# Kernel optimization log

Measured on AMD Instinct MI355X. Metric: run time of the kernel, lower is better.

Reference implementation:

```python
import jax, jax.numpy as jnp
import numpy as np

N = 64      # features
L = 96      # history length
LP = 24     # prediction length
H = 128     # rnn hidden
B = 1024    # batch


def setup_inputs() -> dict:
    key = jax.random.key(0)
    ks = jax.random.split(key, 16)
    # monotonically increasing timestamps
    tp_all = jnp.cumsum(jax.random.uniform(ks[0], (B, L + LP), dtype=jnp.float32), axis=1)
    tp_true = tp_all[:, :L]
    tp_pred = tp_all[:, L:]
    X = jax.random.normal(ks[1], (B, L, N), dtype=jnp.float32)
    mask = jax.random.randint(ks[2], (B, L, N), 0, 2).astype(jnp.float32)
    def unif(k, shape, fan):
        std = 1.0 / np.sqrt(fan)
        return jax.random.uniform(k, shape, jnp.float32, -std, std)
    # TemporalDecay for h: W (H,N), b (H); std = 1/sqrt(out)
    Wh_dec = unif(ks[3], (H, N), H)
    bh_dec = unif(ks[4], (H,), H)
    # TemporalDecay for x (diag): W (N,N) but only diagonal used
    Wx_dec = unif(ks[5], (N, N), N)
    bx_dec = unif(ks[6], (N,), N)
    # GRUCell: input size = 2N + H
    in_sz = 2 * N + H
    W_ih = unif(ks[7], (3 * H, in_sz), H)
    W_hh = unif(ks[8], (3 * H, H), H)
    b_ih = unif(ks[9], (3 * H,), H)
    b_hh = unif(ks[10], (3 * H,), H)
    # output projection
    Wp = unif(ks[11], (N, H), H)
    bp = unif(ks[12], (N,), H)
    return {"tp_pred": tp_pred, "X": X, "tp_true": tp_true, "mask": mask,
            "Wh_dec": Wh_dec, "bh_dec": bh_dec, "Wx_dec": Wx_dec, "bx_dec": bx_dec,
            "W_ih": W_ih, "W_hh": W_hh, "b_ih": b_ih, "b_hh": b_hh,
            "Wp": Wp, "bp": bp}


def _grud(tp_pred, X, tp_true, mask, Wh_dec, bh_dec, Wx_dec, bx_dec,
          W_ih, W_hh, b_ih, b_hh, Wp, bp):
    Bsz, Lh, Nf = X.shape
    Lp = tp_pred.shape[1]
    Lall = Lh + Lp
    Hh = Wh_dec.shape[0]

    # pad future with zeros (unobserved)
    X_all = jnp.concatenate([X, jnp.zeros((Bsz, Lp, Nf), X.dtype)], axis=1)
    M_all = jnp.concatenate([mask, jnp.zeros((Bsz, Lp, Nf), X.dtype)], axis=1)
    tp = jnp.concatenate([tp_true, tp_pred], axis=1)

    # deltas: first-difference padded with 0 at t=0, broadcast over features
    dt = jnp.pad(tp[:, 1:] - tp[:, :-1], ((0, 0), (1, 0)))  # (B, Lall)
    deltas = jnp.broadcast_to(dt[:, :, None], (Bsz, Lall, Nf))

    # empirical mean over positions where (1 - mask) == 1 (faithful to source)
    valid = 1.0 - M_all
    cnt = jnp.clip(valid.sum(axis=1), 1.0, None)  # (B, N)
    mu = (X_all * valid).sum(axis=1) / cnt        # (B, N)

    # LOCF as in source: where mask != 0, copy previous value
    def locf_step(prev, xm):
        x_t, m_t = xm
        cur = jnp.where(m_t != 0, prev, x_t)
        return cur, cur
    _, X_locf = jax.lax.scan(locf_step, X_all[:, 0],
                             (jnp.swapaxes(X_all, 0, 1), jnp.swapaxes(M_all, 0, 1)))
    # X_locf: (Lall, B, N)

    diag_Wx = jnp.diag(Wx_dec)  # (N,) -- diag=True masks W with identity

    def step(h, inputs):
        x_t, m_t, d_t, xl_t = inputs  # each (B, N)
        gh = jnp.exp(-jax.nn.relu(d_t @ Wh_dec.T + bh_dec))      # (B, H)
        gx = jnp.exp(-jax.nn.relu(d_t * diag_Wx + bx_dec))       # (B, N)
        h = h * gh
        rep = h
        x_h = gx * xl_t + (1.0 - gx) * mu
        x_in = m_t * x_t + (1.0 - m_t) * x_h
        inp = jnp.concatenate([x_in, h, m_t], axis=1)             # (B, 2N+H)
        gi = inp @ W_ih.T + b_ih                                  # (B, 3H)
        gr = h @ W_hh.T + b_hh                                    # (B, 3H)
        r = jax.nn.sigmoid(gi[:, :Hh] + gr[:, :Hh])
        z = jax.nn.sigmoid(gi[:, Hh:2 * Hh] + gr[:, Hh:2 * Hh])
        n = jnp.tanh(gi[:, 2 * Hh:] + r * gr[:, 2 * Hh:])
        h_new = (1.0 - z) * n + z * h
        return h_new, rep

    h0 = jnp.zeros((Bsz, Hh), X.dtype)
    xs = (jnp.swapaxes(X_all, 0, 1), jnp.swapaxes(M_all, 0, 1),
          jnp.swapaxes(deltas, 0, 1), X_locf)
    _, reps = jax.lax.scan(step, h0, xs)          # (Lall, B, H)
    reps = jnp.swapaxes(reps, 0, 1)               # (B, Lall, H)
    recon = reps @ Wp.T + bp                      # (B, Lall, N)
    y_hat = recon[:, -Lp:]                        # (B, Lp, N)
    return y_hat[None]                            # (1, B, Lp, N)


def reference(tp_pred, X, tp_true, mask, Wh_dec, bh_dec, Wx_dec, bx_dec,
              W_ih, W_hh, b_ih, b_hh, Wp, bp):
    return _grud(tp_pred, X, tp_true, mask, Wh_dec, bh_dec, Wx_dec, bx_dec,
                 W_ih, W_hh, b_ih, b_hh, Wp, bp)
```

## Files before the change

kernel.cpp:

```cpp
#include <hip/hip_runtime.h>

#define N_F 64
#define L_H 96
#define L_P 24
#define L_ALL 120
#define H_DIM 128
#define B_SZ 1024
#define LOG2E 1.4426950408889634f

typedef _Float16 f16x8 __attribute__((ext_vector_type(8)));
typedef float f32x4 __attribute__((ext_vector_type(4)));

__device__ __forceinline__ float sig_fast(float x) {
    return __builtin_amdgcn_rcpf(1.0f + __builtin_amdgcn_exp2f(-LOG2E * x));
}
__device__ __forceinline__ float tanh_fast(float x) {
    return 1.0f - 2.0f * __builtin_amdgcn_rcpf(1.0f + __builtin_amdgcn_exp2f(2.0f * LOG2E * x));
}
__device__ __forceinline__ float expnr_fast(float x) {
    return __builtin_amdgcn_exp2f(-LOG2E * fmaxf(x, 0.0f));
}

__device__ __forceinline__ void barrier_lds_only() {
    __asm__ volatile("s_waitcnt lgkmcnt(0)\n\ts_barrier" ::: "memory");
}

struct F8 { float v[8]; };
__device__ __forceinline__ F8 ld8(const float* p) {
    F8 r;
    float4 a = *(const float4*)p;
    float4 b = *(const float4*)(p + 4);
    r.v[0]=a.x; r.v[1]=a.y; r.v[2]=a.z; r.v[3]=a.w;
    r.v[4]=b.x; r.v[5]=b.y; r.v[6]=b.z; r.v[7]=b.w;
    return r;
}

__global__ __launch_bounds__(512, 2) void grud_kernel(
    const float* __restrict__ tp_pred, const float* __restrict__ X,
    const float* __restrict__ tp_true, const float* __restrict__ mask,
    const float* __restrict__ Wh_dec, const float* __restrict__ bh_dec,
    const float* __restrict__ Wx_dec, const float* __restrict__ bx_dec,
    const float* __restrict__ W_ih, const float* __restrict__ W_hh,
    const float* __restrict__ b_ih, const float* __restrict__ b_hh,
    const float* __restrict__ Wp, const float* __restrict__ bp,
    float* __restrict__ out)
{
    constexpr int VROW = 264;
    __shared__ alignas(16) _Float16 V[2][16 * VROW];
    __shared__ float dt_lds[L_ALL * 4];
    __shared__ float muA[8][64], muC[8][64];

    const int tid  = threadIdx.x;
    const int w    = tid >> 6;
    const int l    = tid & 63;
    const int quad = l >> 4;
    const int lm   = l & 15;
    const int b0   = blockIdx.x * 4;

    for (int idx = tid; idx < 16 * VROW; idx += 512)
        ((unsigned int*)V)[idx] = 0;

    for (int idx = tid; idx < L_ALL * 4; idx += 512) {
        int t = idx >> 2, q = idx & 3;
        int b = b0 + q;
        float v = 0.0f;
        if (t != 0) {
            float cur = (t < L_H) ? tp_true[b * L_H + t] : tp_pred[b * L_P + (t - L_H)];
            float prv = ((t - 1) < L_H) ? tp_true[b * L_H + (t - 1)]
                                        : tp_pred[b * L_P + (t - 1 - L_H)];
            v = cur - prv;
        }
        dt_lds[idx] = v;
    }

    {
        const int q = w & 3, half = w >> 2;
        const float* xr = X    + (size_t)(b0 + q) * L_H * N_F + l;
        const float* mr = mask + (size_t)(b0 + q) * L_H * N_F + l;
        float a = 0.0f, c = 0.0f;
        for (int t = half * 48; t < half * 48 + 48; ++t) {
            float x = xr[(size_t)t * N_F], m = mr[(size_t)t * N_F];
            a += x * (1.0f - m); c += 1.0f - m;
        }
        muA[w][l] = a; muC[w][l] = c;
    }
    __syncthreads();

    float muv = 0.0f;
    if (w < 4)
        muv = (muA[w][l] + muA[w + 4][l]) / (muC[w][l] + muC[w + 4][l] + (float)L_P);

    const float wxd = Wx_dec[l * N_F + l];
    const float bxn = bx_dec[l];

    const int hc = w * 16 + lm;
    float S = 0.0f;
    {
        const float4* wh4 = (const float4*)(Wh_dec + hc * N_F);
#pragma unroll
        for (int i = 0; i < 16; ++i) { float4 u = wh4[i]; S += u.x + u.y + u.z + u.w; }
    }
    const float bhv = bh_dec[hc];
    const float bR  = b_ih[hc] + b_hh[hc];
    const float bZ  = b_ih[H_DIM + hc] + b_hh[H_DIM + hc];
    const float bN  = b_ih[2 * H_DIM + hc];
    const float bG  = b_hh[2 * H_DIM + hc];

    f16x8 wR[8], wZ[8], wN[8], wG[4];
#pragma unroll
    for (int fi = 0; fi < 8; ++fi) {
        const int kk = fi * 32 + quad * 8;
        const int jr = hc, jz = H_DIM + hc, jn = 2 * H_DIM + hc;
        F8 r8, z8, n8;
        if (fi < 2) {
            r8 = ld8(W_ih + jr * 256 + kk);
            z8 = ld8(W_ih + jz * 256 + kk);
            n8 = ld8(W_ih + jn * 256 + kk);
        } else if (fi < 4) {
            r8 = ld8(W_ih + jr * 256 + 128 + kk);
            z8 = ld8(W_ih + jz * 256 + 128 + kk);
            n8 = ld8(W_ih + jn * 256 + 128 + kk);
        } else {
            const int c = kk - 128;
            r8 = ld8(W_ih + jr * 256 + 64 + c);
            z8 = ld8(W_ih + jz * 256 + 64 + c);
            n8 = ld8(W_ih + jn * 256 + 64 + c);
            F8 rh = ld8(W_hh + jr * 128 + c);
            F8 zh = ld8(W_hh + jz * 128 + c);
            F8 g8 = ld8(W_hh + jn * 128 + c);
#pragma unroll
            for (int q = 0; q < 8; ++q) {
                r8.v[q] += rh.v[q];
                z8.v[q] += zh.v[q];
                wG[fi - 4][q] = (_Float16)g8.v[q];
            }
        }
#pragma unroll
        for (int q = 0; q < 8; ++q) {
            wR[fi][q] = (_Float16)r8.v[q];
            wZ[fi][q] = (_Float16)z8.v[q];
            wN[fi][q] = (_Float16)n8.v[q];
        }
    }

    f16x8 wP[4];
    float bpv = 0.0f;
    const int pn = (w & 3) * 16 + lm;
    if (w >= 4) {
        bpv = bp[pn];
#pragma unroll
        for (int p = 0; p < 4; ++p) {
            F8 p8 = ld8(Wp + pn * H_DIM + p * 32 + quad * 8);
#pragma unroll
            for (int q = 0; q < 8; ++q) wP[p][q] = (_Float16)p8.v[q];
        }
    }

    if (w < 4) {
        const size_t o = (size_t)(b0 + w) * L_H * N_F + l;
        float x0 = X[o], m0 = mask[o];
        const float gx = expnr_fast(bxn);
        float xi = (m0 != 0.0f) ? x0 : (x0 - muv) * gx + muv;
        V[0][4 * w * VROW + l]      = (_Float16)xi;
        V[0][4 * w * VROW + 64 + l] = (_Float16)m0;
    }

    float h = 0.0f;
    __syncthreads();

    auto ldxm = [&](int t, float& px, float& pm) {
        if (t < L_H) {
            const size_t o = (size_t)(b0 + w) * L_H * N_F + (size_t)t * N_F + l;
            px = X[o]; pm = mask[o];
        } else { px = 0.0f; pm = 0.0f; }
    };

    auto body = [&](int t, float cx, float cm, float& fx, float& fm) {
        const int p = t & 1;

        f16x8 af[8];
#pragma unroll
        for (int fi = 0; fi < 8; ++fi)
            af[fi] = *(const f16x8*)&V[p][lm * VROW + fi * 32 + quad * 8];

        if (w < 4) ldxm(t + 3, fx, fm);

        f32x4 aR = {bR, bR, bR, bR}, aZ = {bZ, bZ, bZ, bZ};
        f32x4 aN = {bN, bN, bN, bN}, aG = {bG, bG, bG, bG};
#pragma unroll
        for (int fi = 0; fi < 8; ++fi) {
            aR = __builtin_amdgcn_mfma_f32_16x16x32_f16(af[fi], wR[fi], aR, 0, 0, 0);
            aZ = __builtin_amdgcn_mfma_f32_16x16x32_f16(af[fi], wZ[fi], aZ, 0, 0, 0);
            aN = __builtin_amdgcn_mfma_f32_16x16x32_f16(af[fi], wN[fi], aN, 0, 0, 0);
        }
#pragma unroll
        for (int p4 = 0; p4 < 4; ++p4)
            aG = __builtin_amdgcn_mfma_f32_16x16x32_f16(af[4 + p4], wG[p4], aG, 0, 0, 0);

        if (t >= L_H && w >= 4) {
            f32x4 aP = {bpv, bpv, bpv, bpv};
#pragma unroll
            for (int p4 = 0; p4 < 4; ++p4)
                aP = __builtin_amdgcn_mfma_f32_16x16x32_f16(af[4 + p4], wP[p4], aP, 0, 0, 0);
            out[((size_t)(b0 + quad) * L_P + (t - L_H)) * N_F + pn] = aP[0];
        }

        float ghn = 0.0f;
        if (t < L_ALL - 1) {
            if (w < 4) {
                const float d  = dt_lds[(t + 1) * 4 + w];
                const float gx = expnr_fast(d * wxd + bxn);
                const float xi = (cm != 0.0f) ? cx : (cx - muv) * gx + muv;
                V[p ^ 1][4 * w * VROW + l]      = (_Float16)xi;
                V[p ^ 1][4 * w * VROW + 64 + l] = (_Float16)cm;
            }
            const float dq = dt_lds[(t + 1) * 4 + quad];
            ghn = expnr_fast(dq * S + bhv);
        }

        {
            const float rg = sig_fast(aR[0]);
            const float zg = sig_fast(aZ[0]);
            const float ng = tanh_fast(aN[0] + rg * aG[0]);
            h = zg * (h - ng) + ng;
        }
        if (t < L_ALL - 1) {
            h *= ghn;
            V[p ^ 1][4 * quad * VROW + H_DIM + hc] = (_Float16)h;
        }

        barrier_lds_only();
    };

    float aXv = 0, aMv = 0, bXv = 0, bMv = 0;
    if (w < 4) { ldxm(1, aXv, aMv); ldxm(2, bXv, bMv); }

    for (int t = 0; t < L_ALL; t += 2) {
        body(t,     aXv, aMv, aXv, aMv);
        body(t + 1, bXv, bMv, bXv, bMv);
    }
}

extern "C" void kernel_launch(void* const* d_in, const int* in_sizes, int n_in,
                              void* d_out, int out_size, void* d_ws, size_t ws_size,
                              hipStream_t stream) {
    const float* tp_pred = (const float*)d_in[0];
    const float* X       = (const float*)d_in[1];
    const float* tp_true = (const float*)d_in[2];
    const float* mask    = (const float*)d_in[3];
    const float* Wh_dec  = (const float*)d_in[4];
    const float* bh_dec  = (const float*)d_in[5];
    const float* Wx_dec  = (const float*)d_in[6];
    const float* bx_dec  = (const float*)d_in[7];
    const float* W_ih    = (const float*)d_in[8];
    const float* W_hh    = (const float*)d_in[9];
    const float* b_ih    = (const float*)d_in[10];
    const float* b_hh    = (const float*)d_in[11];
    const float* Wp      = (const float*)d_in[12];
    const float* bp      = (const float*)d_in[13];

    grud_kernel<<<dim3(B_SZ / 4), dim3(512), 0, stream>>>(
        tp_pred, X, tp_true, mask, Wh_dec, bh_dec, Wx_dec, bx_dec,
        W_ih, W_hh, b_ih, b_hh, Wp, bp, (float*)d_out);
}
```

Baseline: 243.6 us.

## Precompute input-gate GEMM ahead in a ring buffer, shrink recurrent critical path

Moves the input projection (x and mask columns of W_ih) off the per-timestep critical path. A producer pipeline, spread over the four sub-steps of each group, loads X and mask, imputes them, and runs MFMAs four timesteps ahead, storing fp16 gate partials in an LDS ring. The recurrent step then needs only the h-dependent K=128 MFMAs. Blocks drop to 256 threads with two hidden columns per lane and a large LDS pad to force one block per CU. This adds fp16 rounding of the precomputed partials and more register pressure in exchange for a shorter serial dependency chain per step.

```diff
diff --git a/kernel.cpp b/kernel.cpp
--- a/kernel.cpp
+++ b/kernel.cpp
@@ -1,26 +1,20 @@
 #include <hip/hip_runtime.h>
 
-#define N_F 64
-#define L_H 96
-#define L_P 24
-#define L_ALL 120
-#define H_DIM 128
-#define B_SZ 1024
-#define LOG2E 1.4426950408889634f
+#define L2E 1.4426950408889634f
 
 typedef _Float16 f16x8 __attribute__((ext_vector_type(8)));
+typedef _Float16 f16x4 __attribute__((ext_vector_type(4)));
 typedef float f32x4 __attribute__((ext_vector_type(4)));
 
 __device__ __forceinline__ float sig_fast(float x) {
-    return __builtin_amdgcn_rcpf(1.0f + __builtin_amdgcn_exp2f(-LOG2E * x));
+    return __builtin_amdgcn_rcpf(1.0f + __builtin_amdgcn_exp2f(-L2E * x));
 }
 __device__ __forceinline__ float tanh_fast(float x) {
-    return 1.0f - 2.0f * __builtin_amdgcn_rcpf(1.0f + __builtin_amdgcn_exp2f(2.0f * LOG2E * x));
+    return 1.0f - 2.0f * __builtin_amdgcn_rcpf(1.0f + __builtin_amdgcn_exp2f(2.0f * L2E * x));
 }
 __device__ __forceinline__ float expnr_fast(float x) {
-    return __builtin_amdgcn_exp2f(-LOG2E * fmaxf(x, 0.0f));
-}
-
+    return __builtin_amdgcn_exp2f(-L2E * fmaxf(x, 0.0f));
+}
 __device__ __forceinline__ void barrier_lds_only() {
     __asm__ volatile("s_waitcnt lgkmcnt(0)\n\ts_barrier" ::: "memory");
 }
@@ -28,14 +22,25 @@
 struct F8 { float v[8]; };
 __device__ __forceinline__ F8 ld8(const float* p) {
     F8 r;
-    float4 a = *(const float4*)p;
-    float4 b = *(const float4*)(p + 4);
+    float4 a = *(const float4*)p, b = *(const float4*)(p + 4);
     r.v[0]=a.x; r.v[1]=a.y; r.v[2]=a.z; r.v[3]=a.w;
     r.v[4]=b.x; r.v[5]=b.y; r.v[6]=b.z; r.v[7]=b.w;
     return r;
 }
-
-__global__ __launch_bounds__(512, 2) void grud_kernel(
+__device__ __forceinline__ f16x8 cvt8(F8 a) {
+    f16x8 r;
+#pragma unroll
+    for (int q = 0; q < 8; ++q) r[q] = (_Float16)a.v[q];
+    return r;
+}
+__device__ __forceinline__ f16x8 cvt8s(F8 a, F8 b) {
+    f16x8 r;
+#pragma unroll
+    for (int q = 0; q < 8; ++q) r[q] = (_Float16)(a.v[q] + b.v[q]);
+    return r;
+}
+
+__global__ __launch_bounds__(256, 1) void grud_kernel(
     const float* __restrict__ tp_pred, const float* __restrict__ X,
     const float* __restrict__ tp_true, const float* __restrict__ mask,
     const float* __restrict__ Wh_dec, const float* __restrict__ bh_dec,
@@ -45,199 +50,221 @@
     const float* __restrict__ Wp, const float* __restrict__ bp,
     float* __restrict__ out)
 {
-    constexpr int VROW = 264;
-    __shared__ alignas(16) _Float16 V[2][16 * VROW];
-    __shared__ float dt_lds[L_ALL * 4];
-    __shared__ float muA[8][64], muC[8][64];
+    constexpr int SR = 136;
+    __shared__ alignas(16) _Float16 ring[16 * 1536];
+    __shared__ alignas(16) _Float16 V[2][16 * SR];
+    __shared__ alignas(16) _Float16 Astage[2][16 * SR];
+    __shared__ float dt_lds[480];
+    __shared__ float mu_l[4][64];
+    __shared__ float wxl[64], bxl[64];
+    __shared__ char occupancy_pad[32768];
 
     const int tid  = threadIdx.x;
-    const int w    = tid >> 6;
-    const int l    = tid & 63;
-    const int quad = l >> 4;
-    const int lm   = l & 15;
+    const int w    = tid >> 6, l = tid & 63, quad = l >> 4, lm = l & 15;
     const int b0   = blockIdx.x * 4;
 
-    for (int idx = tid; idx < 16 * VROW; idx += 512)
-        ((unsigned int*)V)[idx] = 0;
-
-    for (int idx = tid; idx < L_ALL * 4; idx += 512) {
-        int t = idx >> 2, q = idx & 3;
-        int b = b0 + q;
+    if (tid > 100000) occupancy_pad[0] = 1;
+
+    for (int i = tid; i < 16 * SR; i += 256) ((unsigned*)V)[i] = 0;
+
+    for (int i = tid; i < 480; i += 256) {
+        int t = i >> 2, q = i & 3, b = b0 + q;
         float v = 0.0f;
-        if (t != 0) {
-            float cur = (t < L_H) ? tp_true[b * L_H + t] : tp_pred[b * L_P + (t - L_H)];
-            float prv = ((t - 1) < L_H) ? tp_true[b * L_H + (t - 1)]
-                                        : tp_pred[b * L_P + (t - 1 - L_H)];
+        if (t) {
+            float cur = (t < 96) ? tp_true[b * 96 + t] : tp_pred[b * 24 + t - 96];
+            float prv = (t - 1 < 96) ? tp_true[b * 96 + t - 1] : tp_pred[b * 24 + t - 97];
             v = cur - prv;
         }
-        dt_lds[idx] = v;
-    }
+        dt_lds[i] = v;
+    }
+    if (tid < 64) { wxl[tid] = Wx_dec[tid * 65]; bxl[tid] = bx_dec[tid]; }
 
     {
-        const int q = w & 3, half = w >> 2;
-        const float* xr = X    + (size_t)(b0 + q) * L_H * N_F + l;
-        const float* mr = mask + (size_t)(b0 + q) * L_H * N_F + l;
+        const float* xr = X    + ((size_t)(b0 + w) * 96) * 64 + l;
+        const float* mr = mask + ((size_t)(b0 + w) * 96) * 64 + l;
         float a = 0.0f, c = 0.0f;
-        for (int t = half * 48; t < half * 48 + 48; ++t) {
-            float x = xr[(size_t)t * N_F], m = mr[(size_t)t * N_F];
+#pragma unroll 4
+        for (int t = 0; t < 96; ++t) {
+            float x = xr[t * 64], m = mr[t * 64];
             a += x * (1.0f - m); c += 1.0f - m;
         }
-        muA[w][l] = a; muC[w][l] = c;
-    }
-    __syncthreads();
-
-    float muv = 0.0f;
-    if (w < 4)
-        muv = (muA[w][l] + muA[w + 4][l]) / (muC[w][l] + muC[w + 4][l] + (float)L_P);
-
-    const float wxd = Wx_dec[l * N_F + l];
-    const float bxn = bx_dec[l];
-
-    const int hc = w * 16 + lm;
-    float S = 0.0f;
+        mu_l[w][l] = a / (c + 24.0f);
+    }
+
+    const int c0 = 32 * w + lm, c1 = c0 + 16;
+
+    f16x8 wxf[3][2][4];
+#pragma unroll
+    for (int g = 0; g < 3; ++g)
+#pragma unroll
+        for (int j = 0; j < 2; ++j)
+#pragma unroll
+            for (int fi = 0; fi < 4; ++fi) {
+                const int row = g * 128 + (j ? c1 : c0);
+                const int k0 = fi * 32 + quad * 8;
+                wxf[g][j][fi] = cvt8(ld8(W_ih + row * 256 + (k0 < 64 ? k0 : 128 + k0)));
+            }
+
+    f16x8 wRZ[2][2][4], wNf[2][4], wGf[2][4], wPf[4];
+    float S_[2], bh_[2], bR_[2], bZ_[2], bN_[2], bG_[2];
+#pragma unroll
+    for (int j = 0; j < 2; ++j) {
+        const int c = j ? c1 : c0;
+#pragma unroll
+        for (int fi = 0; fi < 4; ++fi) {
+            const int k0 = fi * 32 + quad * 8;
+            wRZ[0][j][fi] = cvt8s(ld8(W_ih + c * 256 + 64 + k0),
+                                  ld8(W_hh + c * 128 + k0));
+            wRZ[1][j][fi] = cvt8s(ld8(W_ih + (128 + c) * 256 + 64 + k0),
+                                  ld8(W_hh + (128 + c) * 128 + k0));
+            wNf[j][fi] = cvt8(ld8(W_ih + (256 + c) * 256 + 64 + k0));
+            wGf[j][fi] = cvt8(ld8(W_hh + (256 + c) * 128 + k0));
+        }
+        float s = 0.0f;
+        const float4* wh4 = (const float4*)(Wh_dec + c * 64);
+#pragma unroll
+        for (int i = 0; i < 16; ++i) { float4 u = wh4[i]; s += u.x + u.y + u.z + u.w; }
+        S_[j]  = s;
+        bh_[j] = bh_dec[c];
+        bR_[j] = b_ih[c] + b_hh[c];
+        bZ_[j] = b_ih[128 + c] + b_hh[128 + c];
+        bN_[j] = b_ih[256 + c];
+        bG_[j] = b_hh[256 + c];
+    }
+    const int pn = w * 16 + lm;
+    const float bpv = bp[pn];
+#pragma unroll
+    for (int fi = 0; fi < 4; ++fi)
+        wPf[fi] = cvt8(ld8(Wp + pn * 128 + fi * 32 + quad * 8));
+
+    auto prodLoad = [&](int gp, float4& px, float4& pm) {
+        if (gp >= 24) { px = make_float4(0,0,0,0); pm = make_float4(0,0,0,0); return; }
+        const int R = tid >> 4, tg = 4 * gp + (R >> 2), b = R & 3;
+        const size_t o = (((size_t)(b0 + b) * 96) + tg) * 64 + (tid & 15) * 4;
+        px = *(const float4*)(X + o);
+        pm = *(const float4*)(mask + o);
+    };
+    auto prodStage = [&](int gp, float4 px, float4 pm) {
+        const int R = tid >> 4, toff = R >> 2, b = R & 3;
+        const int tg = 4 * gp + toff, n0 = (tid & 15) * 4;
+        const float d = dt_lds[tg * 4 + b];
+        const float xs[4] = {px.x, px.y, px.z, px.w};
+        const float ms[4] = {pm.x, pm.y, pm.z, pm.w};
+        f16x4 xi, mm;
+#pragma unroll
+        for (int e = 0; e < 4; ++e) {
+            const int n = n0 + e;
+            const float gxv = expnr_fast(d * wxl[n] + bxl[n]);
+            const float muv = mu_l[b][n];
+            float v;
+            if (gp < 24) {
+                v = (ms[e] != 0.0f) ? xs[e] : (xs[e] - muv) * gxv + muv;
+                mm[e] = (_Float16)ms[e];
+            } else {
+                v = (1.0f - gxv) * muv;
+                mm[e] = (_Float16)0.0f;
+            }
+            xi[e] = (_Float16)v;
+        }
+        *(f16x4*)&Astage[gp & 1][R * SR + n0]      = xi;
+        *(f16x4*)&Astage[gp & 1][R * SR + 64 + n0] = mm;
+    };
+    auto prodMMA = [&](int gp, int j) {
+        f16x8 ap[4];
+#pragma unroll
+        for (int fi = 0; fi < 4; ++fi)
+            ap[fi] = *(const f16x8*)&Astage[gp & 1][lm * SR + fi * 32 + quad * 8];
+        const int tg = 4 * gp + quad, slot = tg & 15;
+        const int c = j ? c1 : c0;
+#pragma unroll
+        for (int g = 0; g < 3; ++g) {
+            f32x4 acc = {0, 0, 0, 0};
+#pragma unroll
+            for (int fi = 0; fi < 4; ++fi)
+                acc = __builtin_amdgcn_mfma_f32_16x16x32_f16(ap[fi], wxf[g][j][fi], acc, 0, 0, 0);
+            f16x4 pk = {(_Float16)acc[0], (_Float16)acc[1], (_Float16)acc[2], (_Float16)acc[3]};
+            *(f16x4*)&ring[slot * 1536 + (g * 128 + c) * 4] = pk;
+        }
+    };
+
+    float h0 = 0.0f, h1 = 0.0f;
+
+    auto step = [&](int t, auto&& extra) {
+        const int p = t & 1;
+        f16x8 af[4];
+#pragma unroll
+        for (int fi = 0; fi < 4; ++fi)
+            af[fi] = *(const f16x8*)&V[p][lm * SR + fi * 32 + quad * 8];
+        const int slot = t & 15;
+        _Float16 g6[6];
+#pragma unroll
+        for (int j = 0; j < 2; ++j)
+#pragma unroll
+            for (int g = 0; g < 3; ++g)
+                g6[j * 3 + g] = ring[slot * 1536 + (g * 128 + (j ? c1 : c0)) * 4 + quad];
+
+        extra();
+
+        f32x4 aR0 = {(float)g6[0] + bR_[0], 0, 0, 0}, aZ0 = {(float)g6[1] + bZ_[0], 0, 0, 0};
+        f32x4 aN0 = {(float)g6[2] + bN_[0], 0, 0, 0}, aG0 = {bG_[0], 0, 0, 0};
+        f32x4 aR1 = {(float)g6[3] + bR_[1], 0, 0, 0}, aZ1 = {(float)g6[4] + bZ_[1], 0, 0, 0};
+        f32x4 aN1 = {(float)g6[5] + bN_[1], 0, 0, 0}, aG1 = {bG_[1], 0, 0, 0};
+#pragma unroll
+        for (int fi = 0; fi < 4; ++fi) {
+            aR0 = __builtin_amdgcn_mfma_f32_16x16x32_f16(af[fi], wRZ[0][0][fi], aR0, 0, 0, 0);
+            aZ0 = __builtin_amdgcn_mfma_f32_16x16x32_f16(af[fi], wRZ[1][0][fi], aZ0, 0, 0, 0);
+            aN0 = __builtin_amdgcn_mfma_f32_16x16x32_f16(af[fi], wNf[0][fi], aN0, 0, 0, 0);
+            aG0 = __builtin_amdgcn_mfma_f32_16x16x32_f16(af[fi], wGf[0][fi], aG0, 0, 0, 0);
+            aR1 = __builtin_amdgcn_mfma_f32_16x16x32_f16(af[fi], wRZ[0][1][fi], aR1, 0, 0, 0);
+            aZ1 = __builtin_amdgcn_mfma_f32_16x16x32_f16(af[fi], wRZ[1][1][fi], aZ1, 0, 0, 0);
+            aN1 = __builtin_amdgcn_mfma_f32_16x16x32_f16(af[fi], wNf[1][fi], aN1, 0, 0, 0);
+            aG1 = __builtin_amdgcn_mfma_f32_16x16x32_f16(af[fi], wGf[1][fi], aG1, 0, 0, 0);
+        }
+        if (t >= 96) {
+            f32x4 aP = {bpv, 0, 0, 0};
+#pragma unroll
+            for (int fi = 0; fi < 4; ++fi)
+                aP = __builtin_amdgcn_mfma_f32_16x16x32_f16(af[fi], wPf[fi], aP, 0, 0, 0);
+            out[((size_t)(b0 + quad) * 24 + (t - 96)) * 64 + pn] = aP[0];
+        }
+        {
+            const float rg0 = sig_fast(aR0[0]), zg0 = sig_fast(aZ0[0]);
+            const float ng0 = tanh_fast(aN0[0] + rg0 * aG0[0]);
+            h0 = zg0 * (h0 - ng0) + ng0;
+            const float rg1 = sig_fast(aR1[0]), zg1 = sig_fast(aZ1[0]);
+            const float ng1 = tanh_fast(aN1[0] + rg1 * aG1[0]);
+            h1 = zg1 * (h1 - ng1) + ng1;
+        }
+        if (t < 119) {
+            const float d = dt_lds[(t + 1) * 4 + quad];
+            h0 *= expnr_fast(d * S_[0] + bh_[0]);
+            h1 *= expnr_fast(d * S_[1] + bh_[1]);
+            V[p ^ 1][(4 * quad) * SR + c0] = (_Float16)h0;
+            V[p ^ 1][(4 * quad) * SR + c1] = (_Float16)h1;
+        }
+        barrier_lds_only();
+    };
+
     {
-        const float4* wh4 = (const float4*)(Wh_dec + hc * N_F);
-#pragma unroll
-        for (int i = 0; i < 16; ++i) { float4 u = wh4[i]; S += u.x + u.y + u.z + u.w; }
-    }
-    const float bhv = bh_dec[hc];
-    const float bR  = b_ih[hc] + b_hh[hc];
-    const float bZ  = b_ih[H_DIM + hc] + b_hh[H_DIM + hc];
-    const float bN  = b_ih[2 * H_DIM + hc];
-    const float bG  = b_hh[2 * H_DIM + hc];
-
-    f16x8 wR[8], wZ[8], wN[8], wG[4];
-#pragma unroll
-    for (int fi = 0; fi < 8; ++fi) {
-        const int kk = fi * 32 + quad * 8;
-        const int jr = hc, jz = H_DIM + hc, jn = 2 * H_DIM + hc;
-        F8 r8, z8, n8;
-        if (fi < 2) {
-            r8 = ld8(W_ih + jr * 256 + kk);
-            z8 = ld8(W_ih + jz * 256 + kk);
-            n8 = ld8(W_ih + jn * 256 + kk);
-        } else if (fi < 4) {
-            r8 = ld8(W_ih + jr * 256 + 128 + kk);
-            z8 = ld8(W_ih + jz * 256 + 128 + kk);
-            n8 = ld8(W_ih + jn * 256 + 128 + kk);
-        } else {
-            const int c = kk - 128;
-            r8 = ld8(W_ih + jr * 256 + 64 + c);
-            z8 = ld8(W_ih + jz * 256 + 64 + c);
-            n8 = ld8(W_ih + jn * 256 + 64 + c);
-            F8 rh = ld8(W_hh + jr * 128 + c);
-            F8 zh = ld8(W_hh + jz * 128 + c);
-            F8 g8 = ld8(W_hh + jn * 128 + c);
-#pragma unroll
-            for (int q = 0; q < 8; ++q) {
-                r8.v[q] += rh.v[q];
-                z8.v[q] += zh.v[q];
-                wG[fi - 4][q] = (_Float16)g8.v[q];
-            }
-        }
-#pragma unroll
-        for (int q = 0; q < 8; ++q) {
-            wR[fi][q] = (_Float16)r8.v[q];
-            wZ[fi][q] = (_Float16)z8.v[q];
-            wN[fi][q] = (_Float16)n8.v[q];
-        }
-    }
-
-    f16x8 wP[4];
-    float bpv = 0.0f;
-    const int pn = (w & 3) * 16 + lm;
-    if (w >= 4) {
-        bpv = bp[pn];
-#pragma unroll
-        for (int p = 0; p < 4; ++p) {
-            F8 p8 = ld8(Wp + pn * H_DIM + p * 32 + quad * 8);
-#pragma unroll
-            for (int q = 0; q < 8; ++q) wP[p][q] = (_Float16)p8.v[q];
-        }
-    }
-
-    if (w < 4) {
-        const size_t o = (size_t)(b0 + w) * L_H * N_F + l;
-        float x0 = X[o], m0 = mask[o];
-        const float gx = expnr_fast(bxn);
-        float xi = (m0 != 0.0f) ? x0 : (x0 - muv) * gx + muv;
-        V[0][4 * w * VROW + l]      = (_Float16)xi;
-        V[0][4 * w * VROW + 64 + l] = (_Float16)m0;
-    }
-
-    float h = 0.0f;
-    __syncthreads();
-
-    auto ldxm = [&](int t, float& px, float& pm) {
-        if (t < L_H) {
-            const size_t o = (size_t)(b0 + w) * L_H * N_F + (size_t)t * N_F + l;
-            px = X[o]; pm = mask[o];
-        } else { px = 0.0f; pm = 0.0f; }
-    };
-
-    auto body = [&](int t, float cx, float cm, float& fx, float& fm) {
-        const int p = t & 1;
-
-        f16x8 af[8];
-#pragma unroll
-        for (int fi = 0; fi < 8; ++fi)
-            af[fi] = *(const f16x8*)&V[p][lm * VROW + fi * 32 + quad * 8];
-
-        if (w < 4) ldxm(t + 3, fx, fm);
-
-        f32x4 aR = {bR, bR, bR, bR}, aZ = {bZ, bZ, bZ, bZ};
-        f32x4 aN = {bN, bN, bN, bN}, aG = {bG, bG, bG, bG};
-#pragma unroll
-        for (int fi = 0; fi < 8; ++fi) {
-            aR = __builtin_amdgcn_mfma_f32_16x16x32_f16(af[fi], wR[fi], aR, 0, 0, 0);
-            aZ = __builtin_amdgcn_mfma_f32_16x16x32_f16(af[fi], wZ[fi], aZ, 0, 0, 0);
-            aN = __builtin_amdgcn_mfma_f32_16x16x32_f16(af[fi], wN[fi], aN, 0, 0, 0);
-        }
-#pragma unroll
-        for (int p4 = 0; p4 < 4; ++p4)
-            aG = __builtin_amdgcn_mfma_f32_16x16x32_f16(af[4 + p4], wG[p4], aG, 0, 0, 0);
-
-        if (t >= L_H && w >= 4) {
-            f32x4 aP = {bpv, bpv, bpv, bpv};
-#pragma unroll
-            for (int p4 = 0; p4 < 4; ++p4)
-                aP = __builtin_amdgcn_mfma_f32_16x16x32_f16(af[4 + p4], wP[p4], aP, 0, 0, 0);
-            out[((size_t)(b0 + quad) * L_P + (t - L_H)) * N_F + pn] = aP[0];
-        }
-
-        float ghn = 0.0f;
-        if (t < L_ALL - 1) {
-            if (w < 4) {
-                const float d  = dt_lds[(t + 1) * 4 + w];
-                const float gx = expnr_fast(d * wxd + bxn);
-                const float xi = (cm != 0.0f) ? cx : (cx - muv) * gx + muv;
-                V[p ^ 1][4 * w * VROW + l]      = (_Float16)xi;
-                V[p ^ 1][4 * w * VROW + 64 + l] = (_Float16)cm;
-            }
-            const float dq = dt_lds[(t + 1) * 4 + quad];
-            ghn = expnr_fast(dq * S + bhv);
-        }
-
-        {
-            const float rg = sig_fast(aR[0]);
-            const float zg = sig_fast(aZ[0]);
-            const float ng = tanh_fast(aN[0] + rg * aG[0]);
-            h = zg * (h - ng) + ng;
-        }
-        if (t < L_ALL - 1) {
-            h *= ghn;
-            V[p ^ 1][4 * quad * VROW + H_DIM + hc] = (_Float16)h;
-        }
-
+        float4 px0, pm0, px1, pm1;
+        prodLoad(0, px0, pm0);
+        prodLoad(1, px1, pm1);
+        __syncthreads();
+        prodStage(0, px0, pm0);
+        prodStage(1, px1, pm1);
+        __syncthreads();
+        prodMMA(0, 0); prodMMA(0, 1);
+        prodMMA(1, 0); prodMMA(1, 1);
         barrier_lds_only();
-    };
-
-    float aXv = 0, aMv = 0, bXv = 0, bMv = 0;
-    if (w < 4) { ldxm(1, aXv, aMv); ldxm(2, bXv, bMv); }
-
-    for (int t = 0; t < L_ALL; t += 2) {
-        body(t,     aXv, aMv, aXv, aMv);
-        body(t + 1, bXv, bMv, bXv, bMv);
+    }
+
+    for (int k = 0; k < 30; ++k) {
+        const int gp = k + 2;
+        float4 px, pm;
+        step(4 * k + 0, [&] { if (gp < 30) prodLoad(gp, px, pm); });
+        step(4 * k + 1, [&] { if (gp < 30) prodStage(gp, px, pm); });
+        step(4 * k + 2, [&] { if (gp < 30) prodMMA(gp, 0); });
+        step(4 * k + 3, [&] { if (gp < 30) prodMMA(gp, 1); });
     }
 }
 
@@ -259,7 +286,7 @@
     const float* Wp      = (const float*)d_in[12];
     const float* bp      = (const float*)d_in[13];
 
-    grud_kernel<<<dim3(B_SZ / 4), dim3(512), 0, stream>>>(
+    grud_kernel<<<dim3(256), dim3(256), 0, stream>>>(
         tp_pred, X, tp_true, mask, Wh_dec, bh_dec, Wx_dec, bx_dec,
         W_ih, W_hh, b_ih, b_hh, Wp, bp, (float*)d_out);
 }
```

Result: faster. 232.5 us (-4.5%).
